# Performance work log

Hardware: AMD Instinct MI355X
Metric: run time of the kernel (lower is better)

Reference implementation:

```python
import jax, jax.numpy as jnp
import numpy as np

N_EMBED = 1024
N_HEADS = 16
CTX = 2048
B, T = 4, 2048
HD = N_EMBED // N_HEADS


def setup_inputs() -> dict:
    key = jax.random.key(0)
    ks = jax.random.split(key, 5)
    scale = 1.0 / np.sqrt(N_EMBED)
    return {
        "x": jax.random.normal(ks[0], (B, T, N_EMBED), dtype=jnp.float32),
        "wq": jax.random.normal(ks[1], (N_EMBED, N_EMBED), dtype=jnp.float32) * scale,
        "wk": jax.random.normal(ks[2], (N_EMBED, N_EMBED), dtype=jnp.float32) * scale,
        "wv": jax.random.normal(ks[3], (N_EMBED, N_EMBED), dtype=jnp.float32) * scale,
        "wo": jax.random.normal(ks[4], (N_EMBED, N_EMBED), dtype=jnp.float32) * scale,
    }


def reference(x, wq, wk, wv, wo):
    b, t, c = x.shape
    # nn.Linear applies x @ W.T ; split heads -> [B, H, T, hd]
    def proj(w):
        return jnp.einsum("btc,dc->btd", x, w).reshape(b, t, N_HEADS, HD).transpose(0, 2, 1, 3)
    q, k, v = proj(wq), proj(wk), proj(wv)
    scores = jnp.einsum("bhqd,bhkd->bhqk", q, k) * (HD ** -0.5)
    causal = jnp.tril(jnp.ones((t, t), dtype=bool))
    scores = jnp.where(causal[None, None, :, :], scores, -jnp.inf)
    a = jax.nn.softmax(scores, axis=-1)
    o = jnp.einsum("bhqk,bhkd->bhqd", a, v)  # [B,H,T,hd]
    o = o.transpose(0, 2, 1, 3).reshape(b, t, c)
    return jnp.einsum("btc,dc->btd", o, wo)
```

## Files before the change

### kernel.cpp

```cpp
#include <hip/hip_runtime.h>
#include <stdint.h>


typedef __attribute__((ext_vector_type(8))) short bf16x8;
typedef __attribute__((ext_vector_type(4))) float f32x4;
typedef unsigned short us;

#define LOG2E 1.4426950408889634f

#define GL2LDS16(g, l)                                                          \
  __builtin_amdgcn_global_load_lds(                                             \
      (const __attribute__((address_space(1))) unsigned int*)(g),               \
      (__attribute__((address_space(3))) unsigned int*)(l), 16, 0, 0)

__device__ inline us f2bf(float f) {
  union { float f; unsigned int u; } v; v.f = f;
  unsigned int u = v.u;
  u += 0x7FFFu + ((u >> 16) & 1u);
  return (us)(u >> 16);
}

__global__ void cast_all(const float* __restrict__ x,
                         const float* __restrict__ w0, const float* __restrict__ w1,
                         const float* __restrict__ w2, const float* __restrict__ w3,
                         us* __restrict__ xb, us* __restrict__ wbuf) {
  int i = (blockIdx.x * blockDim.x + threadIdx.x) * 8;
  const float* src;
  us* dst;
  float sc = 1.0f;
  if (i < (8 << 20)) {
    src = x + i; dst = xb + i;
  } else {
    int j = i - (8 << 20);
    int seg = j >> 20;
    int off = j & ((1 << 20) - 1);
    const float* w = (seg == 0) ? w0 : (seg == 1) ? w1 : (seg == 2) ? w2 : w3;
    if (seg == 0) sc = 0.125f * LOG2E;
    src = w + off; dst = wbuf + j;
  }
  float4 a = *reinterpret_cast<const float4*>(src);
  float4 b = *reinterpret_cast<const float4*>(src + 4);
  union { us u[8]; uint4 v; } o;
  o.u[0] = f2bf(a.x * sc); o.u[1] = f2bf(a.y * sc);
  o.u[2] = f2bf(a.z * sc); o.u[3] = f2bf(a.w * sc);
  o.u[4] = f2bf(b.x * sc); o.u[5] = f2bf(b.y * sc);
  o.u[6] = f2bf(b.z * sc); o.u[7] = f2bf(b.w * sc);
  *reinterpret_cast<uint4*>(dst) = o.v;
}

template <int OUT_BF16>
__global__ __launch_bounds__(256, 2) void gemm_bt(
    const us* __restrict__ A, const us* __restrict__ Bw,
    void* __restrict__ Cv, int M, int N, int K) {
  __shared__ __align__(16) us Al[128 * 64];
  __shared__ __align__(16) us Bl[128 * 64];
  const int tid = threadIdx.x;
  const int lane = tid & 63;
  const int w = tid >> 6;
  const int quad = lane >> 4;
  const int l16 = lane & 15;
  const int m0 = blockIdx.y * 128;
  const int n0 = blockIdx.x * 128;
  const int wm = w >> 1, wn = w & 1;
  const int srow_base = w * 8 + (lane >> 3);
  const int sunit = lane & 7;
  f32x4 acc[4][4] = {};

  for (int k0 = 0; k0 < K; k0 += 64) {
    __syncthreads();
#pragma unroll
    for (int it = 0; it < 4; ++it) {
      int row = it * 32 + srow_base;
      int gu = sunit ^ (row & 7);
      int base = __builtin_amdgcn_readfirstlane((it * 256 + w * 64) * 8);
      GL2LDS16(A + (size_t)(m0 + row) * K + k0 + gu * 8, &Al[base]);
      GL2LDS16(Bw + (size_t)(n0 + row) * K + k0 + gu * 8, &Bl[base]);
    }
    __syncthreads();
#pragma unroll
    for (int kk = 0; kk < 2; ++kk) {
      bf16x8 af[4], bfr[4];
#pragma unroll
      for (int mi = 0; mi < 4; ++mi) {
        int row = wm * 64 + mi * 16 + l16;
        af[mi] = *reinterpret_cast<const bf16x8*>(
            &Al[row * 64 + (((kk * 4 + quad) ^ (row & 7)) * 8)]);
      }
#pragma unroll
      for (int ni = 0; ni < 4; ++ni) {
        int row = wn * 64 + ni * 16 + l16;
        bfr[ni] = *reinterpret_cast<const bf16x8*>(
            &Bl[row * 64 + (((kk * 4 + quad) ^ (row & 7)) * 8)]);
      }
#pragma unroll
      for (int mi = 0; mi < 4; ++mi)
#pragma unroll
        for (int ni = 0; ni < 4; ++ni)
          acc[mi][ni] = __builtin_amdgcn_mfma_f32_16x16x32_bf16(af[mi], bfr[ni], acc[mi][ni], 0, 0, 0);
    }
  }

#pragma unroll
  for (int mi = 0; mi < 4; ++mi)
#pragma unroll
    for (int ni = 0; ni < 4; ++ni)
#pragma unroll
      for (int r = 0; r < 4; ++r) {
        int row = m0 + wm * 64 + mi * 16 + quad * 4 + r;
        int col = n0 + wn * 64 + ni * 16 + l16;
        if (OUT_BF16)
          ((us*)Cv)[(size_t)row * N + col] = f2bf(acc[mi][ni][r]);
        else
          ((float*)Cv)[(size_t)row * N + col] = acc[mi][ni][r];
      }
}

__global__ __launch_bounds__(256) void transpose_v(const us* __restrict__ QKV,
                                                   us* __restrict__ Vt) {
  __shared__ __align__(16) us lds[64 * 80];
  const int bid = blockIdx.x;
  const int kt = bid & 31;
  const int bh = bid >> 5;
  const int b = bh >> 4, h = bh & 15;
  const int tid = threadIdx.x;
#pragma unroll
  for (int it = 0; it < 2; ++it) {
    int u = it * 256 + tid;
    int j = u >> 3;
    int dc = (u & 7) * 8;
    uint4 raw = *reinterpret_cast<const uint4*>(
        &QKV[((size_t)(b * 2048 + kt * 64 + j)) * 3072 + 2048 + h * 64 + dc]);
    us tmp[8];
    *reinterpret_cast<uint4*>(tmp) = raw;
    int sj = (j & 15) * 4 + (j >> 4);
#pragma unroll
    for (int e = 0; e < 8; ++e) lds[(dc + e) * 80 + sj] = tmp[e];
  }
  __syncthreads();
  int d = tid >> 2, c = tid & 3;
  size_t orow = ((size_t)(bh * 64 + d)) * 2048 + kt * 64 + c * 16;
  *reinterpret_cast<uint4*>(&Vt[orow]) = *reinterpret_cast<const uint4*>(&lds[d * 80 + c * 16]);
  *reinterpret_cast<uint4*>(&Vt[orow + 8]) = *reinterpret_cast<const uint4*>(&lds[d * 80 + c * 16 + 8]);
}

__global__ __launch_bounds__(512, 4) void attn(
    const us* __restrict__ QKV, const us* __restrict__ Vt,
    us* __restrict__ O) {
  __shared__ __align__(16) us Kl[64 * 64];
  __shared__ __align__(16) us Vl[64 * 64];
  __shared__ __align__(16) us Pl[8][16 * 64];
  const int bid = blockIdx.x;
  const int pr = bid & 7;
  const int h = (bid >> 3) & 15;
  const int b = bid >> 7;
  const int q0A = pr * 128, q0B = (15 - pr) * 128;
  const int tid = threadIdx.x, lane = tid & 63, w = tid >> 6;
  const int quad = lane >> 4, l16 = lane & 15;
  const size_t rowbase = (size_t)b * 2048;
  const int qcol = h * 64;
  const int kcol = 1024 + h * 64;

  const bf16x8 ones = {(short)0x3F80, (short)0x3F80, (short)0x3F80, (short)0x3F80,
                       (short)0x3F80, (short)0x3F80, (short)0x3F80, (short)0x3F80};

  bf16x8 qfA[2], qfB[2];
#pragma unroll
  for (int dc = 0; dc < 2; ++dc) {
    qfA[dc] = *reinterpret_cast<const bf16x8*>(
        &QKV[(rowbase + q0A + w * 16 + l16) * 3072 + qcol + dc * 32 + quad * 8]);
    qfB[dc] = *reinterpret_cast<const bf16x8*>(
        &QKV[(rowbase + q0B + w * 16 + l16) * 3072 + qcol + dc * 32 + quad * 8]);
  }

  f32x4 oaccA[4] = {}, oaccB[4] = {};
  f32x4 laccA = {}, laccB = {};

  const int rr = tid >> 3;
  const int gu = (tid & 7) ^ (rr & 7);
  const int base = __builtin_amdgcn_readfirstlane(w * 512);
  const int nB = 2 * (15 - pr) + 2;

  auto process = [&](int q0, bf16x8 (&qf)[2], f32x4 (&oacc)[4],
                     f32x4& lacc, int kt) {
    f32x4 s[4] = {};
#pragma unroll
    for (int t = 0; t < 4; ++t) {
      int krow = t * 16 + l16;
#pragma unroll
      for (int dc = 0; dc < 2; ++dc) {
        bf16x8 kf = *reinterpret_cast<const bf16x8*>(
            &Kl[krow * 64 + (((dc * 4 + quad) ^ (l16 & 7)) * 8)]);
        s[t] = __builtin_amdgcn_mfma_f32_16x16x32_bf16(qf[dc], kf, s[t], 0, 0, 0);
      }
    }
    float p[4][4];
    bool do_mask = (kt * 64 + 63) > (q0 + w * 16);
    if (do_mask) {
#pragma unroll
      for (int t = 0; t < 4; ++t)
#pragma unroll
        for (int r = 0; r < 4; ++r) {
          float e = __builtin_amdgcn_exp2f(s[t][r]);
          int kg = kt * 64 + t * 16 + l16;
          int qgl = q0 + w * 16 + quad * 4 + r;
          p[t][r] = (kg <= qgl) ? e : 0.f;
        }
    } else {
#pragma unroll
      for (int t = 0; t < 4; ++t)
#pragma unroll
        for (int r = 0; r < 4; ++r)
          p[t][r] = __builtin_amdgcn_exp2f(s[t][r]);
    }
#pragma unroll
    for (int r = 0; r < 4; ++r) {
      int prow = quad * 4 + r;
      uint2 val;
      val.x = __builtin_amdgcn_perm(__float_as_uint(p[1][r]), __float_as_uint(p[0][r]), 0x07060302u);
      val.y = __builtin_amdgcn_perm(__float_as_uint(p[3][r]), __float_as_uint(p[2][r]), 0x07060302u);
      char* dst = (char*)&Pl[w][0] + prow * 128 +
                  (((l16 >> 1) ^ (prow & 7)) * 16) + (l16 & 1) * 8;
      *reinterpret_cast<uint2*>(dst) = val;
    }
    asm volatile("s_waitcnt lgkmcnt(0)" ::: "memory");
#pragma unroll
    for (int kc = 0; kc < 2; ++kc) {
      bf16x8 pf = *reinterpret_cast<const bf16x8*>(
          (const char*)&Pl[w][0] + l16 * 128 + (((kc * 4 + quad) ^ (l16 & 7)) * 16));
      lacc = __builtin_amdgcn_mfma_f32_16x16x32_bf16(pf, ones, lacc, 0, 0, 0);
#pragma unroll
      for (int dt = 0; dt < 4; ++dt) {
        bf16x8 vf = *reinterpret_cast<const bf16x8*>(
            &Vl[(dt * 16 + l16) * 64 + (((kc * 4 + quad) ^ (l16 & 7)) * 8)]);
        oacc[dt] = __builtin_amdgcn_mfma_f32_16x16x32_bf16(pf, vf, oacc[dt], 0, 0, 0);
      }
    }
  };

  for (int kt = 0; kt < nB; ++kt) {
    __syncthreads();
    GL2LDS16(QKV + (rowbase + kt * 64 + rr) * 3072 + kcol + gu * 8, &Kl[base]);
    GL2LDS16(Vt + ((size_t)((b * 16 + h) * 64 + rr)) * 2048 + kt * 64 + gu * 8, &Vl[base]);
    __syncthreads();
    if (kt * 64 <= q0B + w * 16 + 15) process(q0B, qfB, oaccB, laccB, kt);
    if (kt * 64 <= q0A + w * 16 + 15) process(q0A, qfA, oaccA, laccA, kt);
  }

  auto finalize = [&](int q0, f32x4 (&oacc)[4], f32x4& lacc) {
#pragma unroll
    for (int dt = 0; dt < 4; ++dt)
#pragma unroll
      for (int r = 0; r < 4; ++r) {
        int row = q0 + w * 16 + quad * 4 + r;
        O[(rowbase + row) * 1024 + qcol + dt * 16 + l16] = f2bf(oacc[dt][r] / lacc[r]);
      }
  };
  finalize(q0A, oaccA, laccA);
  finalize(q0B, oaccB, laccB);
}

extern "C" void kernel_launch(void* const* d_in, const int* in_sizes, int n_in,
                              void* d_out, int out_size, void* d_ws, size_t ws_size,
                              hipStream_t stream) {
  const float* x = (const float*)d_in[0];
  const float* wq = (const float*)d_in[1];
  const float* wk = (const float*)d_in[2];
  const float* wv = (const float*)d_in[3];
  const float* wo = (const float*)d_in[4];

  const int BT = 8192, E = 1024;
  const size_t NX = (size_t)BT * E;
  const size_t NW = (size_t)E * E;

  us* xb = (us*)d_ws;
  us* wbuf = xb + NX;
  us* QKV = wbuf + 4 * NW;
  us* VtB = QKV + (size_t)BT * 3 * E;
  us* Ob = xb;

  cast_all<<<(int)((NX + 4 * NW) / 8 / 256), 256, 0, stream>>>(x, wq, wk, wv, wo, xb, wbuf);

  gemm_bt<1><<<dim3(24, 64), 256, 0, stream>>>(xb, wbuf, QKV, BT, 3 * E, E);
  transpose_v<<<64 * 32, 256, 0, stream>>>(QKV, VtB);
  attn<<<4 * 16 * 8, 512, 0, stream>>>(QKV, VtB, Ob);
  gemm_bt<0><<<dim3(8, 64), 256, 0, stream>>>(Ob, wbuf + 3 * NW, (float*)d_out, BT, E, E);
}
```

Measured before the change: 239.3 us.

## Fuse V transpose into QKV GEMM epilogue and split attention into smaller blocks

The QKV projection GEMM now writes V directly in the transposed, permuted layout that attention expects, which removes the separate transpose_v kernel and its extra read and write of V. The attention kernel is reshaped from 512-thread blocks covering 128-row query pairs to 256-thread blocks covering 64-row pairs, doubling the grid to improve load balance and occupancy. The scattered 2-byte Vt stores in the GEMM epilogue are poorly coalesced. Smaller attention blocks also load K/V tiles more times in total.

```diff
diff --git a/kernel.cpp b/kernel.cpp
--- a/kernel.cpp
+++ b/kernel.cpp
@@ -48,10 +48,10 @@
   *reinterpret_cast<uint4*>(dst) = o.v;
 }
 
-template <int OUT_BF16>
-__global__ __launch_bounds__(256, 2) void gemm_bt(
+__global__ __launch_bounds__(256, 2) void gemm_qkv(
     const us* __restrict__ A, const us* __restrict__ Bw,
-    void* __restrict__ Cv, int M, int N, int K) {
+    us* __restrict__ QKV, us* __restrict__ Vt) {
+  const int K = 1024, N = 3072;
   __shared__ __align__(16) us Al[128 * 64];
   __shared__ __align__(16) us Bl[128 * 64];
   const int tid = threadIdx.x;
@@ -100,6 +100,86 @@
     }
   }
 
+  if (n0 < 2048) {
+#pragma unroll
+    for (int mi = 0; mi < 4; ++mi)
+#pragma unroll
+      for (int ni = 0; ni < 4; ++ni)
+#pragma unroll
+        for (int r = 0; r < 4; ++r) {
+          int row = m0 + wm * 64 + mi * 16 + quad * 4 + r;
+          int col = n0 + wn * 64 + ni * 16 + l16;
+          QKV[(size_t)row * N + col] = f2bf(acc[mi][ni][r]);
+        }
+  } else {
+    const int b = m0 >> 11;
+    const int kt = ((m0 & 2047) >> 6) + wm;
+#pragma unroll
+    for (int mi = 0; mi < 4; ++mi)
+#pragma unroll
+      for (int ni = 0; ni < 4; ++ni)
+#pragma unroll
+        for (int r = 0; r < 4; ++r) {
+          int col = n0 + wn * 64 + ni * 16 + l16;
+          int h = (col - 2048) >> 6;
+          int d = col & 63;
+          int sj = (quad * 4 + r) * 4 + mi;
+          Vt[((size_t)((b * 16 + h) * 64 + d)) * 2048 + kt * 64 + sj] = f2bf(acc[mi][ni][r]);
+        }
+  }
+}
+
+__global__ __launch_bounds__(256, 2) void gemm_out(
+    const us* __restrict__ A, const us* __restrict__ Bw,
+    float* __restrict__ Cv, int M, int N, int K) {
+  __shared__ __align__(16) us Al[128 * 64];
+  __shared__ __align__(16) us Bl[128 * 64];
+  const int tid = threadIdx.x;
+  const int lane = tid & 63;
+  const int w = tid >> 6;
+  const int quad = lane >> 4;
+  const int l16 = lane & 15;
+  const int m0 = blockIdx.y * 128;
+  const int n0 = blockIdx.x * 128;
+  const int wm = w >> 1, wn = w & 1;
+  const int srow_base = w * 8 + (lane >> 3);
+  const int sunit = lane & 7;
+  f32x4 acc[4][4] = {};
+
+  for (int k0 = 0; k0 < K; k0 += 64) {
+    __syncthreads();
+#pragma unroll
+    for (int it = 0; it < 4; ++it) {
+      int row = it * 32 + srow_base;
+      int gu = sunit ^ (row & 7);
+      int base = __builtin_amdgcn_readfirstlane((it * 256 + w * 64) * 8);
+      GL2LDS16(A + (size_t)(m0 + row) * K + k0 + gu * 8, &Al[base]);
+      GL2LDS16(Bw + (size_t)(n0 + row) * K + k0 + gu * 8, &Bl[base]);
+    }
+    __syncthreads();
+#pragma unroll
+    for (int kk = 0; kk < 2; ++kk) {
+      bf16x8 af[4], bfr[4];
+#pragma unroll
+      for (int mi = 0; mi < 4; ++mi) {
+        int row = wm * 64 + mi * 16 + l16;
+        af[mi] = *reinterpret_cast<const bf16x8*>(
+            &Al[row * 64 + (((kk * 4 + quad) ^ (row & 7)) * 8)]);
+      }
+#pragma unroll
+      for (int ni = 0; ni < 4; ++ni) {
+        int row = wn * 64 + ni * 16 + l16;
+        bfr[ni] = *reinterpret_cast<const bf16x8*>(
+            &Bl[row * 64 + (((kk * 4 + quad) ^ (row & 7)) * 8)]);
+      }
+#pragma unroll
+      for (int mi = 0; mi < 4; ++mi)
+#pragma unroll
+        for (int ni = 0; ni < 4; ++ni)
+          acc[mi][ni] = __builtin_amdgcn_mfma_f32_16x16x32_bf16(af[mi], bfr[ni], acc[mi][ni], 0, 0, 0);
+    }
+  }
+
 #pragma unroll
   for (int mi = 0; mi < 4; ++mi)
 #pragma unroll
@@ -108,52 +188,21 @@
       for (int r = 0; r < 4; ++r) {
         int row = m0 + wm * 64 + mi * 16 + quad * 4 + r;
         int col = n0 + wn * 64 + ni * 16 + l16;
-        if (OUT_BF16)
-          ((us*)Cv)[(size_t)row * N + col] = f2bf(acc[mi][ni][r]);
-        else
-          ((float*)Cv)[(size_t)row * N + col] = acc[mi][ni][r];
-      }
-}
-
-__global__ __launch_bounds__(256) void transpose_v(const us* __restrict__ QKV,
-                                                   us* __restrict__ Vt) {
-  __shared__ __align__(16) us lds[64 * 80];
-  const int bid = blockIdx.x;
-  const int kt = bid & 31;
-  const int bh = bid >> 5;
-  const int b = bh >> 4, h = bh & 15;
-  const int tid = threadIdx.x;
-#pragma unroll
-  for (int it = 0; it < 2; ++it) {
-    int u = it * 256 + tid;
-    int j = u >> 3;
-    int dc = (u & 7) * 8;
-    uint4 raw = *reinterpret_cast<const uint4*>(
-        &QKV[((size_t)(b * 2048 + kt * 64 + j)) * 3072 + 2048 + h * 64 + dc]);
-    us tmp[8];
-    *reinterpret_cast<uint4*>(tmp) = raw;
-    int sj = (j & 15) * 4 + (j >> 4);
-#pragma unroll
-    for (int e = 0; e < 8; ++e) lds[(dc + e) * 80 + sj] = tmp[e];
-  }
-  __syncthreads();
-  int d = tid >> 2, c = tid & 3;
-  size_t orow = ((size_t)(bh * 64 + d)) * 2048 + kt * 64 + c * 16;
-  *reinterpret_cast<uint4*>(&Vt[orow]) = *reinterpret_cast<const uint4*>(&lds[d * 80 + c * 16]);
-  *reinterpret_cast<uint4*>(&Vt[orow + 8]) = *reinterpret_cast<const uint4*>(&lds[d * 80 + c * 16 + 8]);
-}
-
-__global__ __launch_bounds__(512, 4) void attn(
+        Cv[(size_t)row * N + col] = acc[mi][ni][r];
+      }
+}
+
+__global__ __launch_bounds__(256, 4) void attn(
     const us* __restrict__ QKV, const us* __restrict__ Vt,
     us* __restrict__ O) {
   __shared__ __align__(16) us Kl[64 * 64];
   __shared__ __align__(16) us Vl[64 * 64];
-  __shared__ __align__(16) us Pl[8][16 * 64];
+  __shared__ __align__(16) us Pl[4][16 * 64];
   const int bid = blockIdx.x;
-  const int pr = bid & 7;
-  const int h = (bid >> 3) & 15;
-  const int b = bid >> 7;
-  const int q0A = pr * 128, q0B = (15 - pr) * 128;
+  const int pr = bid & 15;
+  const int h = (bid >> 4) & 15;
+  const int b = bid >> 8;
+  const int q0A = pr * 64, q0B = (31 - pr) * 64;
   const int tid = threadIdx.x, lane = tid & 63, w = tid >> 6;
   const int quad = lane >> 4, l16 = lane & 15;
   const size_t rowbase = (size_t)b * 2048;
@@ -175,10 +224,7 @@
   f32x4 oaccA[4] = {}, oaccB[4] = {};
   f32x4 laccA = {}, laccB = {};
 
-  const int rr = tid >> 3;
-  const int gu = (tid & 7) ^ (rr & 7);
-  const int base = __builtin_amdgcn_readfirstlane(w * 512);
-  const int nB = 2 * (15 - pr) + 2;
+  const int nB = 32 - pr;
 
   auto process = [&](int q0, bf16x8 (&qf)[2], f32x4 (&oacc)[4],
                      f32x4& lacc, int kt) {
@@ -239,8 +285,14 @@
 
   for (int kt = 0; kt < nB; ++kt) {
     __syncthreads();
-    GL2LDS16(QKV + (rowbase + kt * 64 + rr) * 3072 + kcol + gu * 8, &Kl[base]);
-    GL2LDS16(Vt + ((size_t)((b * 16 + h) * 64 + rr)) * 2048 + kt * 64 + gu * 8, &Vl[base]);
+#pragma unroll
+    for (int it = 0; it < 2; ++it) {
+      int row = it * 32 + (tid >> 3);
+      int gu = (tid & 7) ^ (row & 7);
+      int base = __builtin_amdgcn_readfirstlane((it * 32 + w * 8) * 64);
+      GL2LDS16(QKV + (rowbase + kt * 64 + row) * 3072 + kcol + gu * 8, &Kl[base]);
+      GL2LDS16(Vt + ((size_t)((b * 16 + h) * 64 + row)) * 2048 + kt * 64 + gu * 8, &Vl[base]);
+    }
     __syncthreads();
     if (kt * 64 <= q0B + w * 16 + 15) process(q0B, qfB, oaccB, laccB, kt);
     if (kt * 64 <= q0A + w * 16 + 15) process(q0A, qfA, oaccA, laccA, kt);
@@ -280,8 +332,7 @@
 
   cast_all<<<(int)((NX + 4 * NW) / 8 / 256), 256, 0, stream>>>(x, wq, wk, wv, wo, xb, wbuf);
 
-  gemm_bt<1><<<dim3(24, 64), 256, 0, stream>>>(xb, wbuf, QKV, BT, 3 * E, E);
-  transpose_v<<<64 * 32, 256, 0, stream>>>(QKV, VtB);
-  attn<<<4 * 16 * 8, 512, 0, stream>>>(QKV, VtB, Ob);
-  gemm_bt<0><<<dim3(8, 64), 256, 0, stream>>>(Ob, wbuf + 3 * NW, (float*)d_out, BT, E, E);
-}
+  gemm_qkv<<<dim3(24, 64), 256, 0, stream>>>(xb, wbuf, QKV, VtB);
+  attn<<<4 * 16 * 16, 256, 0, stream>>>(QKV, VtB, Ob);
+  gemm_out<<<dim3(8, 64), 256, 0, stream>>>(Ob, wbuf + 3 * NW, (float*)d_out, BT, E, E);
+}
```

Measured after the change: 242.4 us. Within noise of the previous version (+1.3%).
